# Performance work log

Hardware: AMD Instinct MI355X
Metric: run time of the kernel (lower is better)

## Reference

```python
import jax, jax.numpy as jnp
import numpy as np

B, T, D, M = 16, 2048, 512, 1024  # batch, time, input_dim, n_embeddings (groups=1)
TAU = 2.0     # max_temp = curr_temp
ALPHA = -5.0  # self.alpha


def setup_inputs() -> dict:
    key = jax.random.key(0)
    k1, k2, k3 = jax.random.split(key, 3)
    x = jax.random.normal(k1, (B, T, D), dtype=jnp.float32)
    # nn.init.uniform_(embedding, -1, 1); groups=1 so shape (M, D)
    embedding = jax.random.uniform(k2, (M, D), dtype=jnp.float32, minval=-1.0, maxval=1.0)
    # fixed gumbel noise for determinism (torch F.gumbel_softmax samples internally)
    u = jax.random.uniform(k3, (B * T, M), dtype=jnp.float32, minval=1e-6, maxval=1.0 - 1e-6)
    gumbel = -jnp.log(-jnp.log(u))
    return {"x": x, "embedding": embedding, "gumbel": gumbel}


def reference(x, embedding, gumbel):
    bsz, tsz, csz = x.shape
    xf = x.reshape(-1, csz)  # [N, D]
    dist = (jnp.sum(embedding ** 2, axis=1)[None, :]
            + jnp.sum(xf ** 2, axis=1, keepdims=True)
            - 2.0 * (xf @ embedding.T))
    dmap = ALPHA * dist  # [N, M]

    # hard (argmax) one-hot stats
    k = jnp.argmax(dmap, axis=-1)
    hard_x = jax.nn.one_hot(k, M, dtype=dmap.dtype)  # [N, M]
    hard_probs = hard_x.mean(axis=0)
    code_perplexity = -jnp.sum(hard_probs * jnp.log2(hard_probs + 1e-10))
    avg_probs = jax.nn.softmax(dmap, axis=-1).mean(axis=0)
    prob_perplexity = -jnp.sum(avg_probs * jnp.log2(avg_probs + 1e-10))

    # training path: gumbel-softmax with hard=True (straight-through)
    y_soft = jax.nn.softmax((dmap + gumbel) / TAU, axis=-1)
    idx = jnp.argmax(y_soft, axis=-1)
    y_hard = jax.nn.one_hot(idx, M, dtype=y_soft.dtype)
    y = y_hard + y_soft - jax.lax.stop_gradient(y_soft)  # [N, M]

    # weighted embedding sum (groups=1): [N, M] @ [M, D]
    quantized = (y @ embedding).reshape(bsz, tsz, -1)
    commitment_loss = jnp.mean((x - jax.lax.stop_gradient(quantized)) ** 2)
    return quantized, code_perplexity, prob_perplexity, commitment_loss
```

## Files before the change

kernel.cpp:

```cpp
#include <hip/hip_runtime.h>
#include <math.h>

#define NTOT 32768
#define DDIM 512
#define MDIM 1024
#define QOFF 16777216

typedef _Float16 f16x8 __attribute__((ext_vector_type(8)));
typedef float    f32x4 __attribute__((ext_vector_type(4)));

__device__ __forceinline__ void gload_lds16(const void* g, void* l) {
  __builtin_amdgcn_global_load_lds(
      (const __attribute__((address_space(1))) void*)g,
      (__attribute__((address_space(3))) void*)l, 16, 0, 0);
}

__global__ __launch_bounds__(256) void esq_kernel(const float* __restrict__ e,
                                                  float* __restrict__ esq) {
  const int w = threadIdx.x >> 6, lane = threadIdx.x & 63;
  const int m = blockIdx.x * 4 + w;
  const float4* row = (const float4*)(e + (size_t)m * DDIM);
  const float4 a = row[lane * 2];
  const float4 b = row[lane * 2 + 1];
  float s = ((a.x * a.x + a.y * a.y) + (a.z * a.z + a.w * a.w)) +
            ((b.x * b.x + b.y * b.y) + (b.z * b.z + b.w * b.w));
#pragma unroll
  for (int off = 32; off; off >>= 1) s += __shfl_xor(s, off);
  if (lane == 0) esq[m] = s;
}

__global__ __launch_bounds__(256) void e_to_frag(const float* __restrict__ e,
                                                 _Float16* __restrict__ hi,
                                                 _Float16* __restrict__ lo) {
  const int tid = blockIdx.x * 256 + threadIdx.x;
  const int lane = tid & 63;
  const int F = tid >> 6;
  const int mt = F >> 7;
  const int ks = (F >> 3) & 15;
  const int ctg = F & 7;
  const int m = mt * 128 + ctg * 16 + (lane & 15);
  const int k0 = ks * 32 + (lane >> 4) * 8;
  const float* src = e + (size_t)m * DDIM + k0;
  const float4 a = *(const float4*)src;
  const float4 b = *(const float4*)(src + 4);
  f16x8 vh, vl;
  vh[0] = (_Float16)a.x; vl[0] = (_Float16)(a.x - (float)vh[0]);
  vh[1] = (_Float16)a.y; vl[1] = (_Float16)(a.y - (float)vh[1]);
  vh[2] = (_Float16)a.z; vl[2] = (_Float16)(a.z - (float)vh[2]);
  vh[3] = (_Float16)a.w; vl[3] = (_Float16)(a.w - (float)vh[3]);
  vh[4] = (_Float16)b.x; vl[4] = (_Float16)(b.x - (float)vh[4]);
  vh[5] = (_Float16)b.y; vl[5] = (_Float16)(b.y - (float)vh[5]);
  vh[6] = (_Float16)b.z; vl[6] = (_Float16)(b.z - (float)vh[6]);
  vh[7] = (_Float16)b.w; vl[7] = (_Float16)(b.w - (float)vh[7]);
  *(f16x8*)(hi + (size_t)tid * 8) = vh;
  *(f16x8*)(lo + (size_t)tid * 8) = vl;
}

#define CVT1(RT, J, V)                                                         \
  Ah[RT][J] = (_Float16)(V);                                                   \
  Al[RT][J] = (_Float16)((V) - (float)Ah[RT][J]);
#define CVT8(RT, A0, A1)                                                       \
  CVT1(RT, 0, A0[0]) CVT1(RT, 1, A0[1]) CVT1(RT, 2, A0[2]) CVT1(RT, 3, A0[3]) \
  CVT1(RT, 4, A1[0]) CVT1(RT, 5, A1[1]) CVT1(RT, 6, A1[2]) CVT1(RT, 7, A1[3])

#define STAGE(AsP, BhP, BlP, KS)                                               \
  {                                                                            \
    _Pragma("unroll") for (int i_ = 0; i_ < 4; ++i_) {                         \
      const int row_ = (w * 4 + i_) * 8 + (lane >> 3);                         \
      const int cf_ = ((lane & 7) ^ (row_ & 7)) * 4;                           \
      gload_lds16(x + (size_t)(n0 + row_) * DDIM + (KS) * 32 + cf_,            \
                  (AsP) + (w * 4 + i_) * 1024);                                \
    }                                                                          \
    _Pragma("unroll") for (int i_ = 0; i_ < 2; ++i_) {                         \
      const size_t so_ =                                                       \
          (size_t)(mt * 16 + (KS)) * 8192 + (w * 2 + i_) * 1024 + lane * 16;   \
      gload_lds16((const char*)ehi + so_, (BhP) + (w * 2 + i_) * 1024);        \
      gload_lds16((const char*)elo + so_, (BlP) + (w * 2 + i_) * 1024);        \
    }                                                                          \
  }

#define COMPUTE(AsP, BhP, BlP)                                                 \
  {                                                                            \
    f16x8 Bhf[8], Blf[8];                                                      \
    _Pragma("unroll") for (int c_ = 0; c_ < 8; ++c_) {                         \
      Bhf[c_] = *(const f16x8*)((BhP) + c_ * 1024 + lane * 16);                \
      Blf[c_] = *(const f16x8*)((BlP) + c_ * 1024 + lane * 16);                \
    }                                                                          \
    f16x8 Ah[2], Al[2];                                                        \
    _Pragma("unroll") for (int rt_ = 0; rt_ < 2; ++rt_) {                      \
      const int row_ = w * 32 + rt_ * 16 + l15;                                \
      const int sw_ = (row_ & 7) << 4;                                         \
      const char* rb_ = (AsP) + row_ * 128;                                    \
      const f32x4 a0_ = *(const f32x4*)(rb_ + ((lg * 32) ^ sw_));              \
      const f32x4 a1_ = *(const f32x4*)(rb_ + ((lg * 32 + 16) ^ sw_));         \
      CVT8(rt_, a0_, a1_)                                                      \
    }                                                                          \
    _Pragma("unroll") for (int c_ = 0; c_ < 8; ++c_)                           \
        _Pragma("unroll") for (int rt_ = 0; rt_ < 2; ++rt_)                    \
            acc[rt_][c_] = __builtin_amdgcn_mfma_f32_16x16x32_f16(             \
                Ah[rt_], Bhf[c_], acc[rt_][c_], 0, 0, 0);                      \
    _Pragma("unroll") for (int c_ = 0; c_ < 8; ++c_)                           \
        _Pragma("unroll") for (int rt_ = 0; rt_ < 2; ++rt_)                    \
            acc[rt_][c_] = __builtin_amdgcn_mfma_f32_16x16x32_f16(             \
                Al[rt_], Bhf[c_], acc[rt_][c_], 0, 0, 0);                      \
    _Pragma("unroll") for (int c_ = 0; c_ < 8; ++c_)                           \
        _Pragma("unroll") for (int rt_ = 0; rt_ < 2; ++rt_)                    \
            acc[rt_][c_] = __builtin_amdgcn_mfma_f32_16x16x32_f16(             \
                Ah[rt_], Blf[c_], acc[rt_][c_], 0, 0, 0);                      \
  }

__global__ __launch_bounds__(256, 2)
void gemm_dmap(const float* __restrict__ x, const _Float16* __restrict__ ehi,
               const _Float16* __restrict__ elo, const float* __restrict__ esq,
               float* __restrict__ dmap) {
  __shared__ __align__(16) char smem[66048];
  char* const AsA = smem;
  char* const AsB = smem + 16384;
  char* const BhA = smem + 32768;
  char* const BhB = smem + 40960;
  char* const BlA = smem + 49152;
  char* const BlB = smem + 57344;
  float* const esqt = (float*)(smem + 65536);

  const int t = threadIdx.x;
  const int w = t >> 6;
  const int lane = t & 63;
  const int l15 = lane & 15;
  const int lg = lane >> 4;
  const int mt = blockIdx.x & 7;
  const int nt = blockIdx.x >> 3;
  const int n0 = nt * 128;

  if (t < 128) esqt[t] = esq[mt * 128 + t];

  f32x4 acc[2][8];
#pragma unroll
  for (int rt = 0; rt < 2; ++rt)
#pragma unroll
    for (int c = 0; c < 8; ++c) acc[rt][c] = (f32x4){0.f, 0.f, 0.f, 0.f};

  STAGE(AsA, BhA, BlA, 0)
  __syncthreads();

  for (int kk = 0; kk < 8; ++kk) {
    const int ks = kk * 2;
    STAGE(AsB, BhB, BlB, ks + 1)
    COMPUTE(AsA, BhA, BlA)
    __syncthreads();
    if (ks + 2 < 16) STAGE(AsA, BhA, BlA, ks + 2)
    COMPUTE(AsB, BhB, BlB)
    __syncthreads();
  }

#pragma unroll
  for (int rt = 0; rt < 2; ++rt)
#pragma unroll
    for (int ct = 0; ct < 8; ++ct) {
      const float e5 = 5.f * esqt[ct * 16 + l15];
      float* dr = dmap + (size_t)(n0 + w * 32 + rt * 16 + lg * 4) * 1024 +
                  mt * 128 + ct * 16 + l15;
#pragma unroll
      for (int rg = 0; rg < 4; ++rg)
        dr[(size_t)rg * 1024] = 10.f * acc[rt][ct][rg] - e5;
    }
}

#define AMAX(V, MM)                                                            \
  { const float v_ = (V); const int m_ = (MM);                                 \
    if (v_ > bv || (v_ == bv && m_ < bi)) { bv = v_; bi = m_; } }
#define GMAX(V, MM)                                                            \
  { const float v_ = (V); const int m_ = (MM);                                 \
    if (v_ > gv || (v_ == gv && m_ < gi)) { gv = v_; gi = m_; } }

__global__ __launch_bounds__(256)
void epi(const float* __restrict__ x, const float* __restrict__ emb,
         const float* __restrict__ dmap, const float* __restrict__ gum,
         float* __restrict__ out, float* __restrict__ avg_acc,
         int* __restrict__ counts, float* __restrict__ sse) {
  __shared__ float avg_s[MDIM];
  const int t = threadIdx.x;
  const int w = t >> 6;
  const int lane = t & 63;
  const int co = lane << 2;
  avg_s[t] = 0.f; avg_s[t + 256] = 0.f; avg_s[t + 512] = 0.f; avg_s[t + 768] = 0.f;
  __syncthreads();

  float4 cav0 = make_float4(0.f, 0.f, 0.f, 0.f);
  float4 cav1 = make_float4(0.f, 0.f, 0.f, 0.f);
  float4 cav2 = make_float4(0.f, 0.f, 0.f, 0.f);
  float4 cav3 = make_float4(0.f, 0.f, 0.f, 0.f);
  float ss_wave = 0.f;

  for (int i = 0; i < 8; ++i) {
    const int n = blockIdx.x * 32 + w * 8 + i;
    const float* Dr = dmap + (size_t)n * MDIM;
    const float4* grow = (const float4*)(gum + (size_t)n * MDIM);
    const float4 q0 = grow[lane];
    const float4 q1 = grow[lane + 64];
    const float4 q2 = grow[lane + 128];
    const float4 q3 = grow[lane + 192];
    const float4 d0 = *(const float4*)&Dr[co];
    const float4 d1 = *(const float4*)&Dr[co + 256];
    const float4 d2 = *(const float4*)&Dr[co + 512];
    const float4 d3 = *(const float4*)&Dr[co + 768];

    float bv = -3.402823466e+38f; int bi = 0;
    AMAX(d0.x, co + 0)   AMAX(d0.y, co + 1)   AMAX(d0.z, co + 2)   AMAX(d0.w, co + 3)
    AMAX(d1.x, co + 256) AMAX(d1.y, co + 257) AMAX(d1.z, co + 258) AMAX(d1.w, co + 259)
    AMAX(d2.x, co + 512) AMAX(d2.y, co + 513) AMAX(d2.z, co + 514) AMAX(d2.w, co + 515)
    AMAX(d3.x, co + 768) AMAX(d3.y, co + 769) AMAX(d3.z, co + 770) AMAX(d3.w, co + 771)
#pragma unroll
    for (int off = 32; off; off >>= 1) {
      const float ov = __shfl_xor(bv, off);
      const int oi = __shfl_xor(bi, off);
      if (ov > bv || (ov == bv && oi < bi)) { bv = ov; bi = oi; }
    }
    if (lane == 0) atomicAdd(&counts[bi], 1);

    float4 p0, p1, p2, p3;
    p0.x = __expf(d0.x - bv); p0.y = __expf(d0.y - bv); p0.z = __expf(d0.z - bv); p0.w = __expf(d0.w - bv);
    p1.x = __expf(d1.x - bv); p1.y = __expf(d1.y - bv); p1.z = __expf(d1.z - bv); p1.w = __expf(d1.w - bv);
    p2.x = __expf(d2.x - bv); p2.y = __expf(d2.y - bv); p2.z = __expf(d2.z - bv); p2.w = __expf(d2.w - bv);
    p3.x = __expf(d3.x - bv); p3.y = __expf(d3.y - bv); p3.z = __expf(d3.z - bv); p3.w = __expf(d3.w - bv);
    float ssum = (((p0.x + p0.y) + (p0.z + p0.w)) + ((p1.x + p1.y) + (p1.z + p1.w))) +
                 (((p2.x + p2.y) + (p2.z + p2.w)) + ((p3.x + p3.y) + (p3.z + p3.w)));
#pragma unroll
    for (int off = 32; off; off >>= 1) ssum += __shfl_xor(ssum, off);
    const float inv = 1.0f / ssum;
    cav0.x += p0.x * inv; cav0.y += p0.y * inv; cav0.z += p0.z * inv; cav0.w += p0.w * inv;
    cav1.x += p1.x * inv; cav1.y += p1.y * inv; cav1.z += p1.z * inv; cav1.w += p1.w * inv;
    cav2.x += p2.x * inv; cav2.y += p2.y * inv; cav2.z += p2.z * inv; cav2.w += p2.w * inv;
    cav3.x += p3.x * inv; cav3.y += p3.y * inv; cav3.z += p3.z * inv; cav3.w += p3.w * inv;

    float gv = -3.402823466e+38f; int gi = 0;
    GMAX(d0.x + q0.x, co + 0)   GMAX(d0.y + q0.y, co + 1)
    GMAX(d0.z + q0.z, co + 2)   GMAX(d0.w + q0.w, co + 3)
    GMAX(d1.x + q1.x, co + 256) GMAX(d1.y + q1.y, co + 257)
    GMAX(d1.z + q1.z, co + 258) GMAX(d1.w + q1.w, co + 259)
    GMAX(d2.x + q2.x, co + 512) GMAX(d2.y + q2.y, co + 513)
    GMAX(d2.z + q2.z, co + 514) GMAX(d2.w + q2.w, co + 515)
    GMAX(d3.x + q3.x, co + 768) GMAX(d3.y + q3.y, co + 769)
    GMAX(d3.z + q3.z, co + 770) GMAX(d3.w + q3.w, co + 771)
#pragma unroll
    for (int off = 32; off; off >>= 1) {
      const float ov = __shfl_xor(gv, off);
      const int oi = __shfl_xor(gi, off);
      if (ov > gv || (ov == gv && oi < gi)) { gv = ov; gi = oi; }
    }

    const float4* erow = (const float4*)(emb + (size_t)gi * DDIM);
    const float4* xrow = (const float4*)(x + (size_t)n * DDIM);
    float4* orow = (float4*)(out + (size_t)n * DDIM);
#pragma unroll
    for (int c2 = 0; c2 < 2; ++c2) {
      const int f = lane + 64 * c2;
      const float4 ev = erow[f];
      const float4 xv = xrow[f];
      orow[f] = ev;
      const float q0_ = xv.x - ev.x, q1_ = xv.y - ev.y;
      const float q2_ = xv.z - ev.z, q3_ = xv.w - ev.w;
      ss_wave += (q0_ * q0_ + q1_ * q1_) + (q2_ * q2_ + q3_ * q3_);
    }
  }

#pragma unroll
  for (int off = 32; off; off >>= 1) ss_wave += __shfl_xor(ss_wave, off);
  if (lane == 0) atomicAdd(sse, ss_wave);

  atomicAdd(&avg_s[co + 0], cav0.x);   atomicAdd(&avg_s[co + 1], cav0.y);
  atomicAdd(&avg_s[co + 2], cav0.z);   atomicAdd(&avg_s[co + 3], cav0.w);
  atomicAdd(&avg_s[co + 256], cav1.x); atomicAdd(&avg_s[co + 257], cav1.y);
  atomicAdd(&avg_s[co + 258], cav1.z); atomicAdd(&avg_s[co + 259], cav1.w);
  atomicAdd(&avg_s[co + 512], cav2.x); atomicAdd(&avg_s[co + 513], cav2.y);
  atomicAdd(&avg_s[co + 514], cav2.z); atomicAdd(&avg_s[co + 515], cav2.w);
  atomicAdd(&avg_s[co + 768], cav3.x); atomicAdd(&avg_s[co + 769], cav3.y);
  atomicAdd(&avg_s[co + 770], cav3.z); atomicAdd(&avg_s[co + 771], cav3.w);
  __syncthreads();
  atomicAdd(&avg_acc[t], avg_s[t]);
  atomicAdd(&avg_acc[t + 256], avg_s[t + 256]);
  atomicAdd(&avg_acc[t + 512], avg_s[t + 512]);
  atomicAdd(&avg_acc[t + 768], avg_s[t + 768]);
}

__global__ __launch_bounds__(1024)
void finalize(const float* __restrict__ avg_acc, const int* __restrict__ counts,
              const float* __restrict__ sse, float* __restrict__ out) {
  __shared__ float red[32];
  const int t = threadIdx.x;
  const float invN = 1.f / 32768.f;
  const float p = (float)counts[t] * invN;
  float a = p * log2f(p + 1e-10f);
  const float q = avg_acc[t] * invN;
  float b = q * log2f(q + 1e-10f);
#pragma unroll
  for (int off = 32; off; off >>= 1) {
    a += __shfl_xor(a, off);
    b += __shfl_xor(b, off);
  }
  const int wv = t >> 6, ln = t & 63;
  if (ln == 0) { red[wv] = a; red[wv + 16] = b; }
  __syncthreads();
  if (t == 0) {
    float sa = 0.f, sb = 0.f;
#pragma unroll
    for (int i = 0; i < 16; ++i) { sa += red[i]; sb += red[i + 16]; }
    out[QOFF + 0] = -sa;
    out[QOFF + 1] = -sb;
    out[QOFF + 2] = sse[0] * (1.f / (32768.f * 512.f));
  }
}

extern "C" void kernel_launch(void* const* d_in, const int* in_sizes, int n_in,
                              void* d_out, int out_size, void* d_ws,
                              size_t ws_size, hipStream_t stream) {
  const float* x = (const float*)d_in[0];
  const float* e = (const float*)d_in[1];
  const float* g = (const float*)d_in[2];
  float* out = (float*)d_out;
  char* wsb = (char*)d_ws;
  float* esq = (float*)wsb;
  float* avg_acc = (float*)(wsb + 4096);
  int* counts = (int*)(wsb + 8192);
  float* sse = (float*)(wsb + 12288);
  _Float16* ehi = (_Float16*)(wsb + 16384);
  _Float16* elo = (_Float16*)(wsb + 16384 + 1048576);
  float* dmap = (float*)(wsb + 16384 + 2097152);

  const size_t cap = (ws_size > 2113536) ? ws_size - 2113536 : 0;
  long long cr = (long long)(cap / 4096);
  cr = (cr / 128) * 128;
  if (cr > NTOT) cr = NTOT;
  if (cr < 128) cr = 128;
  const int chunk_rows = (int)cr;

  hipMemsetAsync(wsb + 4096, 0, 8192 + 16, stream);

  e_to_frag<<<256, 256, 0, stream>>>(e, ehi, elo);
  esq_kernel<<<256, 256, 0, stream>>>(e, esq);

  for (int n0 = 0; n0 < NTOT; n0 += chunk_rows) {
    const int rows = (NTOT - n0 < chunk_rows) ? (NTOT - n0) : chunk_rows;
    gemm_dmap<<<8 * (rows / 128), 256, 0, stream>>>(
        x + (size_t)n0 * DDIM, ehi, elo, esq, dmap);
    epi<<<rows / 32, 256, 0, stream>>>(
        x + (size_t)n0 * DDIM, e, dmap, g + (size_t)n0 * MDIM,
        out + (size_t)n0 * DDIM, avg_acc, counts, sse);
  }
  finalize<<<1, 1024, 0, stream>>>(avg_acc, counts, sse, out);
}
```

Measured before the change: 243.4 us.

## Derive commitment loss from selected dmap values and software-pipeline epilogue rows

The epilogue no longer reads x rows to compute the squared error. Instead it carries the dmap value at the gumbel-argmax index through the reduction. The commitment SSE is then reconstructed algebraically as sum||x||^2 minus 0.2 times the sum of selected dmap values, with sum||x||^2 coming from a separate streaming xsq kernel. Each wave now handles 4 rows with explicit double-buffered loads of dmap and gumbel, and the grid is doubled. The subtraction of two large sums in fp32 risks cancellation error in the loss, and the fp16-split GEMM error now feeds into that loss directly.

Measured after the change: 328.2 us. 1.35x slower.

```diff
diff --git a/kernel.cpp b/kernel.cpp
--- a/kernel.cpp
+++ b/kernel.cpp
@@ -27,6 +27,21 @@
 #pragma unroll
   for (int off = 32; off; off >>= 1) s += __shfl_xor(s, off);
   if (lane == 0) esq[m] = s;
+}
+
+__global__ __launch_bounds__(256)
+void xsq_kernel(const float* __restrict__ x, float* __restrict__ xsq_tot) {
+  const int tid = blockIdx.x * 256 + threadIdx.x;
+  const float4* xv = (const float4*)x;
+  float s = 0.f;
+#pragma unroll
+  for (int i = 0; i < 16; ++i) {
+    const float4 a = xv[(size_t)i * 262144 + tid];
+    s += (a.x * a.x + a.y * a.y) + (a.z * a.z + a.w * a.w);
+  }
+#pragma unroll
+  for (int off = 32; off; off >>= 1) s += __shfl_xor(s, off);
+  if ((threadIdx.x & 63) == 0) atomicAdd(xsq_tot, s);
 }
 
 __global__ __launch_bounds__(256) void e_to_frag(const float* __restrict__ e,
@@ -168,15 +183,82 @@
 #define AMAX(V, MM)                                                            \
   { const float v_ = (V); const int m_ = (MM);                                 \
     if (v_ > bv || (v_ == bv && m_ < bi)) { bv = v_; bi = m_; } }
-#define GMAX(V, MM)                                                            \
+#define GMAXD(V, MM, DV)                                                       \
   { const float v_ = (V); const int m_ = (MM);                                 \
-    if (v_ > gv || (v_ == gv && m_ < gi)) { gv = v_; gi = m_; } }
+    if (v_ > gv || (v_ == gv && m_ < gi)) { gv = v_; gi = m_; dv = (DV); } }
+
+#define LOADROW(N, D0, D1, D2, D3, Q0, Q1, Q2, Q3)                             \
+  {                                                                            \
+    const float* Dr_ = dmap + (size_t)(N)*MDIM;                                \
+    const float4* Gr_ = (const float4*)(gum + (size_t)(N)*MDIM);               \
+    Q0 = Gr_[lane]; Q1 = Gr_[lane + 64];                                       \
+    Q2 = Gr_[lane + 128]; Q3 = Gr_[lane + 192];                                \
+    D0 = *(const float4*)&Dr_[co];       D1 = *(const float4*)&Dr_[co + 256];  \
+    D2 = *(const float4*)&Dr_[co + 512]; D3 = *(const float4*)&Dr_[co + 768];  \
+  }
+
+#define PROCESS(N, D0, D1, D2, D3, Q0, Q1, Q2, Q3)                             \
+  {                                                                            \
+    float bv = -3.402823466e+38f; int bi = 0;                                  \
+    AMAX(D0.x, co + 0)   AMAX(D0.y, co + 1)   AMAX(D0.z, co + 2)   AMAX(D0.w, co + 3)   \
+    AMAX(D1.x, co + 256) AMAX(D1.y, co + 257) AMAX(D1.z, co + 258) AMAX(D1.w, co + 259) \
+    AMAX(D2.x, co + 512) AMAX(D2.y, co + 513) AMAX(D2.z, co + 514) AMAX(D2.w, co + 515) \
+    AMAX(D3.x, co + 768) AMAX(D3.y, co + 769) AMAX(D3.z, co + 770) AMAX(D3.w, co + 771) \
+    _Pragma("unroll") for (int off = 32; off; off >>= 1) {                     \
+      const float ov = __shfl_xor(bv, off);                                    \
+      const int oi = __shfl_xor(bi, off);                                      \
+      if (ov > bv || (ov == bv && oi < bi)) { bv = ov; bi = oi; }              \
+    }                                                                          \
+    if (lane == 0) atomicAdd(&counts[bi], 1);                                  \
+    float4 p0, p1, p2, p3;                                                     \
+    p0.x = __expf(D0.x - bv); p0.y = __expf(D0.y - bv);                        \
+    p0.z = __expf(D0.z - bv); p0.w = __expf(D0.w - bv);                        \
+    p1.x = __expf(D1.x - bv); p1.y = __expf(D1.y - bv);                        \
+    p1.z = __expf(D1.z - bv); p1.w = __expf(D1.w - bv);                        \
+    p2.x = __expf(D2.x - bv); p2.y = __expf(D2.y - bv);                        \
+    p2.z = __expf(D2.z - bv); p2.w = __expf(D2.w - bv);                        \
+    p3.x = __expf(D3.x - bv); p3.y = __expf(D3.y - bv);                        \
+    p3.z = __expf(D3.z - bv); p3.w = __expf(D3.w - bv);                        \
+    float ssum = (((p0.x + p0.y) + (p0.z + p0.w)) + ((p1.x + p1.y) + (p1.z + p1.w))) + \
+                 (((p2.x + p2.y) + (p2.z + p2.w)) + ((p3.x + p3.y) + (p3.z + p3.w)));  \
+    _Pragma("unroll") for (int off = 32; off; off >>= 1)                       \
+        ssum += __shfl_xor(ssum, off);                                         \
+    const float inv = 1.0f / ssum;                                             \
+    cav0.x += p0.x * inv; cav0.y += p0.y * inv;                                \
+    cav0.z += p0.z * inv; cav0.w += p0.w * inv;                                \
+    cav1.x += p1.x * inv; cav1.y += p1.y * inv;                                \
+    cav1.z += p1.z * inv; cav1.w += p1.w * inv;                                \
+    cav2.x += p2.x * inv; cav2.y += p2.y * inv;                                \
+    cav2.z += p2.z * inv; cav2.w += p2.w * inv;                                \
+    cav3.x += p3.x * inv; cav3.y += p3.y * inv;                                \
+    cav3.z += p3.z * inv; cav3.w += p3.w * inv;                                \
+    float gv = -3.402823466e+38f, dv = 0.f; int gi = 0;                        \
+    GMAXD(D0.x + Q0.x, co + 0, D0.x)     GMAXD(D0.y + Q0.y, co + 1, D0.y)      \
+    GMAXD(D0.z + Q0.z, co + 2, D0.z)     GMAXD(D0.w + Q0.w, co + 3, D0.w)      \
+    GMAXD(D1.x + Q1.x, co + 256, D1.x)   GMAXD(D1.y + Q1.y, co + 257, D1.y)    \
+    GMAXD(D1.z + Q1.z, co + 258, D1.z)   GMAXD(D1.w + Q1.w, co + 259, D1.w)    \
+    GMAXD(D2.x + Q2.x, co + 512, D2.x)   GMAXD(D2.y + Q2.y, co + 513, D2.y)    \
+    GMAXD(D2.z + Q2.z, co + 514, D2.z)   GMAXD(D2.w + Q2.w, co + 515, D2.w)    \
+    GMAXD(D3.x + Q3.x, co + 768, D3.x)   GMAXD(D3.y + Q3.y, co + 769, D3.y)    \
+    GMAXD(D3.z + Q3.z, co + 770, D3.z)   GMAXD(D3.w + Q3.w, co + 771, D3.w)    \
+    _Pragma("unroll") for (int off = 32; off; off >>= 1) {                     \
+      const float ov = __shfl_xor(gv, off);                                    \
+      const int oi = __shfl_xor(gi, off);                                      \
+      const float od = __shfl_xor(dv, off);                                    \
+      if (ov > gv || (ov == gv && oi < gi)) { gv = ov; gi = oi; dv = od; }     \
+    }                                                                          \
+    sd_wave += dv;                                                             \
+    const float4* erow = (const float4*)(emb + (size_t)gi * DDIM);             \
+    float4* orow = (float4*)(out + (size_t)(N)*DDIM);                          \
+    orow[lane] = erow[lane];                                                   \
+    orow[lane + 64] = erow[lane + 64];                                         \
+  }
 
 __global__ __launch_bounds__(256)
-void epi(const float* __restrict__ x, const float* __restrict__ emb,
-         const float* __restrict__ dmap, const float* __restrict__ gum,
-         float* __restrict__ out, float* __restrict__ avg_acc,
-         int* __restrict__ counts, float* __restrict__ sse) {
+void epi(const float* __restrict__ emb, const float* __restrict__ dmap,
+         const float* __restrict__ gum, float* __restrict__ out,
+         float* __restrict__ avg_acc, int* __restrict__ counts,
+         float* __restrict__ sd_acc) {
   __shared__ float avg_s[MDIM];
   const int t = threadIdx.x;
   const int w = t >> 6;
@@ -189,83 +271,22 @@
   float4 cav1 = make_float4(0.f, 0.f, 0.f, 0.f);
   float4 cav2 = make_float4(0.f, 0.f, 0.f, 0.f);
   float4 cav3 = make_float4(0.f, 0.f, 0.f, 0.f);
-  float ss_wave = 0.f;
-
-  for (int i = 0; i < 8; ++i) {
-    const int n = blockIdx.x * 32 + w * 8 + i;
-    const float* Dr = dmap + (size_t)n * MDIM;
-    const float4* grow = (const float4*)(gum + (size_t)n * MDIM);
-    const float4 q0 = grow[lane];
-    const float4 q1 = grow[lane + 64];
-    const float4 q2 = grow[lane + 128];
-    const float4 q3 = grow[lane + 192];
-    const float4 d0 = *(const float4*)&Dr[co];
-    const float4 d1 = *(const float4*)&Dr[co + 256];
-    const float4 d2 = *(const float4*)&Dr[co + 512];
-    const float4 d3 = *(const float4*)&Dr[co + 768];
-
-    float bv = -3.402823466e+38f; int bi = 0;
-    AMAX(d0.x, co + 0)   AMAX(d0.y, co + 1)   AMAX(d0.z, co + 2)   AMAX(d0.w, co + 3)
-    AMAX(d1.x, co + 256) AMAX(d1.y, co + 257) AMAX(d1.z, co + 258) AMAX(d1.w, co + 259)
-    AMAX(d2.x, co + 512) AMAX(d2.y, co + 513) AMAX(d2.z, co + 514) AMAX(d2.w, co + 515)
-    AMAX(d3.x, co + 768) AMAX(d3.y, co + 769) AMAX(d3.z, co + 770) AMAX(d3.w, co + 771)
-#pragma unroll
-    for (int off = 32; off; off >>= 1) {
-      const float ov = __shfl_xor(bv, off);
-      const int oi = __shfl_xor(bi, off);
-      if (ov > bv || (ov == bv && oi < bi)) { bv = ov; bi = oi; }
-    }
-    if (lane == 0) atomicAdd(&counts[bi], 1);
-
-    float4 p0, p1, p2, p3;
-    p0.x = __expf(d0.x - bv); p0.y = __expf(d0.y - bv); p0.z = __expf(d0.z - bv); p0.w = __expf(d0.w - bv);
-    p1.x = __expf(d1.x - bv); p1.y = __expf(d1.y - bv); p1.z = __expf(d1.z - bv); p1.w = __expf(d1.w - bv);
-    p2.x = __expf(d2.x - bv); p2.y = __expf(d2.y - bv); p2.z = __expf(d2.z - bv); p2.w = __expf(d2.w - bv);
-    p3.x = __expf(d3.x - bv); p3.y = __expf(d3.y - bv); p3.z = __expf(d3.z - bv); p3.w = __expf(d3.w - bv);
-    float ssum = (((p0.x + p0.y) + (p0.z + p0.w)) + ((p1.x + p1.y) + (p1.z + p1.w))) +
-                 (((p2.x + p2.y) + (p2.z + p2.w)) + ((p3.x + p3.y) + (p3.z + p3.w)));
-#pragma unroll
-    for (int off = 32; off; off >>= 1) ssum += __shfl_xor(ssum, off);
-    const float inv = 1.0f / ssum;
-    cav0.x += p0.x * inv; cav0.y += p0.y * inv; cav0.z += p0.z * inv; cav0.w += p0.w * inv;
-    cav1.x += p1.x * inv; cav1.y += p1.y * inv; cav1.z += p1.z * inv; cav1.w += p1.w * inv;
-    cav2.x += p2.x * inv; cav2.y += p2.y * inv; cav2.z += p2.z * inv; cav2.w += p2.w * inv;
-    cav3.x += p3.x * inv; cav3.y += p3.y * inv; cav3.z += p3.z * inv; cav3.w += p3.w * inv;
-
-    float gv = -3.402823466e+38f; int gi = 0;
-    GMAX(d0.x + q0.x, co + 0)   GMAX(d0.y + q0.y, co + 1)
-    GMAX(d0.z + q0.z, co + 2)   GMAX(d0.w + q0.w, co + 3)
-    GMAX(d1.x + q1.x, co + 256) GMAX(d1.y + q1.y, co + 257)
-    GMAX(d1.z + q1.z, co + 258) GMAX(d1.w + q1.w, co + 259)
-    GMAX(d2.x + q2.x, co + 512) GMAX(d2.y + q2.y, co + 513)
-    GMAX(d2.z + q2.z, co + 514) GMAX(d2.w + q2.w, co + 515)
-    GMAX(d3.x + q3.x, co + 768) GMAX(d3.y + q3.y, co + 769)
-    GMAX(d3.z + q3.z, co + 770) GMAX(d3.w + q3.w, co + 771)
-#pragma unroll
-    for (int off = 32; off; off >>= 1) {
-      const float ov = __shfl_xor(gv, off);
-      const int oi = __shfl_xor(gi, off);
-      if (ov > gv || (ov == gv && oi < gi)) { gv = ov; gi = oi; }
-    }
-
-    const float4* erow = (const float4*)(emb + (size_t)gi * DDIM);
-    const float4* xrow = (const float4*)(x + (size_t)n * DDIM);
-    float4* orow = (float4*)(out + (size_t)n * DDIM);
-#pragma unroll
-    for (int c2 = 0; c2 < 2; ++c2) {
-      const int f = lane + 64 * c2;
-      const float4 ev = erow[f];
-      const float4 xv = xrow[f];
-      orow[f] = ev;
-      const float q0_ = xv.x - ev.x, q1_ = xv.y - ev.y;
-      const float q2_ = xv.z - ev.z, q3_ = xv.w - ev.w;
-      ss_wave += (q0_ * q0_ + q1_ * q1_) + (q2_ * q2_ + q3_ * q3_);
-    }
-  }
-
-#pragma unroll
-  for (int off = 32; off; off >>= 1) ss_wave += __shfl_xor(ss_wave, off);
-  if (lane == 0) atomicAdd(sse, ss_wave);
+  float sd_wave = 0.f;
+
+  const int nb = blockIdx.x * 16 + w * 4;
+  float4 a0, a1, a2, a3, aq0, aq1, aq2, aq3;
+  float4 b0, b1, b2, b3, bq0, bq1, bq2, bq3;
+
+  LOADROW(nb + 0, a0, a1, a2, a3, aq0, aq1, aq2, aq3)
+  LOADROW(nb + 1, b0, b1, b2, b3, bq0, bq1, bq2, bq3)
+  PROCESS(nb + 0, a0, a1, a2, a3, aq0, aq1, aq2, aq3)
+  LOADROW(nb + 2, a0, a1, a2, a3, aq0, aq1, aq2, aq3)
+  PROCESS(nb + 1, b0, b1, b2, b3, bq0, bq1, bq2, bq3)
+  LOADROW(nb + 3, b0, b1, b2, b3, bq0, bq1, bq2, bq3)
+  PROCESS(nb + 2, a0, a1, a2, a3, aq0, aq1, aq2, aq3)
+  PROCESS(nb + 3, b0, b1, b2, b3, bq0, bq1, bq2, bq3)
+
+  if (lane == 0) atomicAdd(sd_acc, sd_wave);
 
   atomicAdd(&avg_s[co + 0], cav0.x);   atomicAdd(&avg_s[co + 1], cav0.y);
   atomicAdd(&avg_s[co + 2], cav0.z);   atomicAdd(&avg_s[co + 3], cav0.w);
@@ -284,7 +305,8 @@
 
 __global__ __launch_bounds__(1024)
 void finalize(const float* __restrict__ avg_acc, const int* __restrict__ counts,
-              const float* __restrict__ sse, float* __restrict__ out) {
+              const float* __restrict__ sd_acc, const float* __restrict__ xsq,
+              float* __restrict__ out) {
   __shared__ float red[32];
   const int t = threadIdx.x;
   const float invN = 1.f / 32768.f;
@@ -306,7 +328,8 @@
     for (int i = 0; i < 16; ++i) { sa += red[i]; sb += red[i + 16]; }
     out[QOFF + 0] = -sa;
     out[QOFF + 1] = -sb;
-    out[QOFF + 2] = sse[0] * (1.f / (32768.f * 512.f));
+    const float sse = xsq[0] - sd_acc[0] * 0.2f;
+    out[QOFF + 2] = sse * (1.f / (32768.f * 512.f));
   }
 }
 
@@ -321,7 +344,8 @@
   float* esq = (float*)wsb;
   float* avg_acc = (float*)(wsb + 4096);
   int* counts = (int*)(wsb + 8192);
-  float* sse = (float*)(wsb + 12288);
+  float* sd_acc = (float*)(wsb + 12288);
+  float* xsq = (float*)(wsb + 12292);
   _Float16* ehi = (_Float16*)(wsb + 16384);
   _Float16* elo = (_Float16*)(wsb + 16384 + 1048576);
   float* dmap = (float*)(wsb + 16384 + 2097152);
@@ -333,18 +357,19 @@
   if (cr < 128) cr = 128;
   const int chunk_rows = (int)cr;
 
-  hipMemsetAsync(wsb + 4096, 0, 8192 + 16, stream);
+  hipMemsetAsync(wsb + 4096, 0, 8192 + 32, stream);
 
   e_to_frag<<<256, 256, 0, stream>>>(e, ehi, elo);
   esq_kernel<<<256, 256, 0, stream>>>(e, esq);
+  xsq_kernel<<<1024, 256, 0, stream>>>(x, xsq);
 
   for (int n0 = 0; n0 < NTOT; n0 += chunk_rows) {
     const int rows = (NTOT - n0 < chunk_rows) ? (NTOT - n0) : chunk_rows;
     gemm_dmap<<<8 * (rows / 128), 256, 0, stream>>>(
         x + (size_t)n0 * DDIM, ehi, elo, esq, dmap);
-    epi<<<rows / 32, 256, 0, stream>>>(
-        x + (size_t)n0 * DDIM, e, dmap, g + (size_t)n0 * MDIM,
-        out + (size_t)n0 * DDIM, avg_acc, counts, sse);
-  }
-  finalize<<<1, 1024, 0, stream>>>(avg_acc, counts, sse, out);
-}
+    epi<<<rows / 16, 256, 0, stream>>>(
+        e, dmap, g + (size_t)n0 * MDIM, out + (size_t)n0 * DDIM,
+        avg_acc, counts, sd_acc);
+  }
+  finalize<<<1, 1024, 0, stream>>>(avg_acc, counts, sd_acc, xsq, out);
+}
```
